# Optimization experiments

Measured on AMD Instinct MI355X. Metric: run time of the kernel, lower is better.

## Reference

```python
import jax, jax.numpy as jnp
import numpy as np

E = 1024
H = 16
DH = E // H
LN_EPS = 1e-5


def setup_inputs() -> dict:
    key = jax.random.key(0)
    ks = jax.random.split(key, 9)
    B, Lq, Lk = 8, 1024, 1024
    s = 0.02
    return {
        "query": jax.random.normal(ks[0], (B, Lq, E), jnp.float32),
        "key_t": jax.random.normal(ks[1], (B, Lk, E), jnp.float32),
        "value": jax.random.normal(ks[2], (B, Lk, E), jnp.float32),
        "in_proj_w": jax.random.normal(ks[3], (3 * E, E), jnp.float32) * s,
        "in_proj_b": jnp.zeros((3 * E,), jnp.float32),
        "out_proj_w": jax.random.normal(ks[4], (E, E), jnp.float32) * s,
        "out_proj_b": jnp.zeros((E,), jnp.float32),
        "ln_gamma": jnp.ones((E,), jnp.float32),
        "ln_beta": jnp.zeros((E,), jnp.float32),
    }


def _mha_cross(query, key_t, value, in_proj_w, in_proj_b, out_proj_w, out_proj_b,
               ln_gamma, ln_beta):
    B, Lq, _ = query.shape
    Lk = key_t.shape[1]
    wq, wk, wv = in_proj_w[:E], in_proj_w[E:2 * E], in_proj_w[2 * E:]
    bq, bk, bv = in_proj_b[:E], in_proj_b[E:2 * E], in_proj_b[2 * E:]
    # projections (torch Linear: x @ W^T + b)
    q = (query @ wq.T + bq).reshape(B, Lq, H, DH)
    k = (key_t @ wk.T + bk).reshape(B, Lk, H, DH)
    v = (value @ wv.T + bv).reshape(B, Lk, H, DH)
    scale = 1.0 / np.sqrt(DH).astype(np.float32)
    # unfused attention: explicit [B,H,Lq,Lk] scores (need_weights=True path)
    scores = jnp.einsum("bqhd,bkhd->bhqk", q, k) * scale
    probs = jax.nn.softmax(scores, axis=-1)
    attn = jnp.einsum("bhqk,bkhd->bqhd", probs, v).reshape(B, Lq, E)
    attn_out = attn @ out_proj_w.T + out_proj_b
    # averaged attention weights (average_attn_weights=True default)
    attn_weights = probs.mean(axis=1)  # [B, Lq, Lk]
    # residual + LayerNorm
    x = query + attn_out
    mu = x.mean(axis=-1, keepdims=True)
    var = x.var(axis=-1, keepdims=True)
    y = (x - mu) * jax.lax.rsqrt(var + LN_EPS) * ln_gamma + ln_beta
    return y, attn_weights


def reference(query, key_t, value, in_proj_w, in_proj_b, out_proj_w, out_proj_b,
              ln_gamma, ln_beta):
    return _mha_cross(query, key_t, value, in_proj_w, in_proj_b,
                      out_proj_w, out_proj_b, ln_gamma, ln_beta)
```

## Files before the change

kernel.cpp:

```cpp
#include <hip/hip_runtime.h>
#include <stdint.h>

#define E_DIM 1024
#define H_NUM 16
#define B_NUM 8
#define LQ 1024
#define LK 1024
#define MROWS (B_NUM * LQ)

typedef unsigned short u16;
typedef __attribute__((ext_vector_type(8))) short bf16x8;
typedef __attribute__((ext_vector_type(4))) short bf16x4;
typedef __attribute__((ext_vector_type(4))) float f32x4;
typedef bf16x8 __attribute__((may_alias)) bf16x8_ma;
typedef bf16x4 __attribute__((may_alias)) bf16x4_ma;
typedef f32x4 __attribute__((may_alias)) f32x4_ma;

typedef __attribute__((address_space(1))) const void* gas_ptr;
typedef __attribute__((address_space(3))) void* las_ptr;

__device__ __forceinline__ void gload16(const void* g, void* l) {
  __builtin_amdgcn_global_load_lds((gas_ptr)g, (las_ptr)l, 16, 0, 0);
}

__device__ __forceinline__ u16 f2bf(float f) {
  union { float f; uint32_t u; } c; c.f = f;
  return (u16)((c.u + 0x7FFFu + ((c.u >> 16) & 1u)) >> 16);
}

#define MFMA_BF16(a, b, c) __builtin_amdgcn_mfma_f32_16x16x32_bf16((a), (b), (c), 0, 0, 0)

#define SCALE_Q 0.18033688011112042f

__global__ __launch_bounds__(256) void cvt_f32_bf16(const float* __restrict__ src,
                                                    u16* __restrict__ dst, int n4) {
  int i = blockIdx.x * 256 + threadIdx.x;
  const int stride = gridDim.x * 256;
  for (; i < n4; i += stride) {
    float4 v = ((const float4*)src)[i];
    ushort4 o;
    o.x = f2bf(v.x); o.y = f2bf(v.y); o.z = f2bf(v.z); o.w = f2bf(v.w);
    ((ushort4*)dst)[i] = o;
  }
}

__global__ __launch_bounds__(256) void cvt3_f32_bf16(
    const float* __restrict__ a0, const float* __restrict__ a1, const float* __restrict__ a2,
    u16* __restrict__ o0, u16* __restrict__ o1, u16* __restrict__ o2, int n4) {
  const float* s = (blockIdx.y == 0) ? a0 : (blockIdx.y == 1 ? a1 : a2);
  u16* d = (blockIdx.y == 0) ? o0 : (blockIdx.y == 1 ? o1 : o2);
  int i = blockIdx.x * 256 + threadIdx.x;
  const int stride = gridDim.x * 256;
  for (; i < n4; i += stride) {
    float4 v = ((const float4*)s)[i];
    ushort4 o;
    o.x = f2bf(v.x); o.y = f2bf(v.y); o.z = f2bf(v.z); o.w = f2bf(v.w);
    ((ushort4*)d)[i] = o;
  }
}


#define BAR() __builtin_amdgcn_s_barrier()
#define LGKM0() do { asm volatile("s_waitcnt lgkmcnt(0)" ::: "memory"); \
                     __builtin_amdgcn_sched_barrier(0); } while (0)
#define LGKM8() asm volatile("s_waitcnt lgkmcnt(8)" ::: "memory")
#define VMC(n) asm volatile("s_waitcnt vmcnt(" n ")" ::: "memory")

#define STAGEH(mat, rowbase, kt, ldsoff)                                     \
  { const u16* _s = (mat) + (size_t)(rowbase) * E_DIM + (kt);                \
    gload16(_s + goff0, ldsv + (ldsoff) + wave * 1024);                      \
    gload16(_s + goff1, ldsv + (ldsoff) + 8192 + wave * 1024); }

#define READ_B(db)                                                           \
  _Pragma("unroll") for (int n = 0; n < 4; ++n) {                            \
    const int rgb = wn4 + n;                                                 \
    _Pragma("unroll") for (int ks = 0; ks < 2; ++ks)                         \
      bfr[n][ks] = *(const bf16x8_ma*)(ldsc + 65536 + (db) * 32768 +         \
          ((rgb >> 3) << 14) + (((rgb & 7) * 2 + ks) << 10) + lanebase);     \
  }

#define READ_A(db, q)                                                        \
  _Pragma("unroll") for (int jj = 0; jj < 2; ++jj) {                         \
    const int rga = 4 * (q) + 2 * jj + wm;                                   \
    _Pragma("unroll") for (int ks = 0; ks < 2; ++ks)                         \
      afr[jj][ks] = *(const bf16x8_ma*)(ldsc + (db) * 32768 +                \
          ((rga >> 3) << 14) + (((rga & 7) * 2 + ks) << 10) + lanebase);     \
  }

#define MMA(q)                                                               \
  __builtin_amdgcn_s_setprio(1);                                             \
  _Pragma("unroll") for (int jj = 0; jj < 2; ++jj)                           \
    _Pragma("unroll") for (int n = 0; n < 4; ++n)                            \
      _Pragma("unroll") for (int ks = 0; ks < 2; ++ks)                       \
        acc[2 * (q) + jj][n] =                                               \
            MFMA_BF16(afr[jj][ks], bfr[n][ks], acc[2 * (q) + jj][n]);        \
  __builtin_amdgcn_s_setprio(0);

template <int MODE>
__global__ __launch_bounds__(512, 2) void gemm256(
    const u16* __restrict__ A0, const u16* __restrict__ A1, const u16* __restrict__ A2,
    const u16* __restrict__ W, const float* __restrict__ bias,
    const float* __restrict__ resid,
    u16* __restrict__ outb, float* __restrict__ outf,
    int nwg_n, int nwg_m) {
  __shared__ u16 lds[65536];

  const int tid = threadIdx.x;
  const int wave = tid >> 6, lane = tid & 63;
  const int lr = lane & 15, lg = lane >> 4;
  const int wm = wave >> 2, wn4 = (wave & 3) * 4;

  const int cpx = (int)gridDim.x >> 3;
  const int bid = blockIdx.x;
  const int wg = (bid & 7) * cpx + (bid >> 3);
  const int n_i = wg % nwg_n;
  const int rest = wg / nwg_n;
  const int m_i = rest % nwg_m;
  const int z = rest / nwg_m;
  const int m0 = m_i * 256, n0 = n_i * 256;

  const u16* Az = (z == 0) ? A0 : (z == 1 ? A1 : A2);
  const u16* Wz = W + (size_t)z * E_DIM * E_DIM;
  const float* bs = bias + z * E_DIM;
  const float scale = (MODE == 0 && z == 0) ? SCALE_Q : 1.0f;

  int goff0, goff1;
  {
    const int X0 = wave * 1024 + lane * 16;
    const int L0 = X0 ^ (((X0 >> 9) & 1) << 5);
    goff0 = (((L0 >> 10) >> 1) * 16 + ((L0 >> 6) & 15)) * E_DIM +
            ((L0 >> 10) & 1) * 32 + ((L0 & 63) >> 1);
    const int X1 = 8192 + X0;
    const int L1 = X1 ^ (((X1 >> 9) & 1) << 5);
    goff1 = (((L1 >> 10) >> 1) * 16 + ((L1 >> 6) & 15)) * E_DIM +
            ((L1 >> 10) & 1) * 32 + ((L1 & 63) >> 1);
  }
  const char* ldsc = (const char*)lds;
  char* ldsv = (char*)lds;
  const int lanebase = lr * 64 + ((lg * 16) ^ ((lane & 8) << 2));

  const f32x4 fzero = {0.f, 0.f, 0.f, 0.f};
  f32x4 acc[8][4];
#pragma unroll
  for (int j = 0; j < 8; ++j)
#pragma unroll
    for (int n = 0; n < 4; ++n) acc[j][n] = fzero;

  STAGEH(Az, m0,       0,  0);
  STAGEH(Az, m0 + 128, 0,  16384);
  STAGEH(Wz, n0,       0,  65536);
  STAGEH(Wz, n0 + 128, 0,  65536 + 16384);
  STAGEH(Wz, n0,       64, 65536 + 32768);
  STAGEH(Wz, n0 + 128, 64, 65536 + 32768 + 16384);
  STAGEH(Az, m0,       64, 32768);
  VMC("6");
  BAR();

  bf16x8 bfr[4][2], afr[2][2];
#pragma unroll 1
  for (int i = 0; i < 8; ++i) {
    const int kt2 = i * 128 + 128;
    const bool nl = (i < 7);
    READ_B(0) READ_A(0, 0)
    STAGEH(Az, m0 + 128, i * 128 + 64, 32768 + 16384);
    LGKM8();
    BAR(); LGKM0();
    MMA(0)
    BAR();
    READ_A(0, 1)
    if (nl) STAGEH(Wz, n0, kt2, 65536);
    BAR(); LGKM0();
    MMA(1)
    BAR();
    READ_A(0, 2)
    if (nl) STAGEH(Az, m0, kt2, 0);
    BAR(); LGKM0();
    MMA(2)
    BAR();
    READ_A(0, 3)
    if (nl) {
      STAGEH(Wz, n0 + 128, kt2, 65536 + 16384);
      VMC("6");
    } else {
      VMC("0");
    }
    BAR(); LGKM0();
    MMA(3)
    BAR();
    READ_B(1) READ_A(1, 0)
    if (nl) STAGEH(Az, m0 + 128, kt2, 16384);
    LGKM8();
    BAR(); LGKM0();
    MMA(0)
    BAR();
    READ_A(1, 1)
    if (nl) STAGEH(Wz, n0, kt2 + 64, 65536 + 32768);
    BAR(); LGKM0();
    MMA(1)
    BAR();
    READ_A(1, 2)
    if (nl) STAGEH(Wz, n0 + 128, kt2 + 64, 65536 + 32768 + 16384);
    BAR(); LGKM0();
    MMA(2)
    BAR();
    READ_A(1, 3)
    if (nl) {
      STAGEH(Az, m0, kt2 + 64, 32768);
      VMC("6");
    }
    BAR(); LGKM0();
    MMA(3)
    BAR();
  }

  float bvv[4];
#pragma unroll
  for (int n = 0; n < 4; ++n) bvv[n] = bs[n0 + wn4 * 16 + n * 16 + lr];

  if (MODE == 0) {
    u16* Cb = outb + (size_t)z * (size_t)MROWS * E_DIM;
#pragma unroll
    for (int j = 0; j < 8; ++j) {
      const int rbase = m0 + (2 * j + wm) * 16 + lg * 4;
#pragma unroll
      for (int ii = 0; ii < 4; ++ii) {
        const size_t m = (size_t)(rbase + ii);
#pragma unroll
        for (int n = 0; n < 4; ++n) {
          const int nn = n0 + wn4 * 16 + n * 16 + lr;
          Cb[m * E_DIM + nn] = f2bf((acc[j][n][ii] + bvv[n]) * scale);
        }
      }
    }
  } else {
#pragma unroll
    for (int j = 0; j < 8; ++j) {
      const int rbase = m0 + (2 * j + wm) * 16 + lg * 4;
#pragma unroll
      for (int ii = 0; ii < 4; ++ii) {
        const size_t m = (size_t)(rbase + ii);
#pragma unroll
        for (int n = 0; n < 4; ++n) {
          const int nn = n0 + wn4 * 16 + n * 16 + lr;
          outf[m * E_DIM + nn] = acc[j][n][ii] + bvv[n] + resid[m * E_DIM + nn];
        }
      }
    }
  }
}

__global__ __launch_bounds__(256) void gemm128_out(
    const u16* __restrict__ A, const u16* __restrict__ W,
    const float* __restrict__ bias, const float* __restrict__ resid,
    float* __restrict__ outf, int nwg_n, int nwg_m) {
  __shared__ u16 As[128 * 64];
  __shared__ u16 Bs[128 * 64];

  const int tid = threadIdx.x;
  const int wave = tid >> 6;
  const int lane = tid & 63;
  const int lr = lane & 15, lg = lane >> 4;
  const int wr = wave >> 1, wc = wave & 1;

  const int cpx = (int)gridDim.x >> 3;
  const int bid = blockIdx.x;
  const int wg = (bid & 7) * cpx + (bid >> 3);
  const int n_i = wg % nwg_n;
  const int m_i = (wg / nwg_n) % nwg_m;

  const int m0 = m_i * 128;
  const int n0 = n_i * 128;

  const f32x4 fzero = {0.f, 0.f, 0.f, 0.f};
  f32x4 acc[4][4];
#pragma unroll
  for (int a = 0; a < 4; ++a)
#pragma unroll
    for (int b = 0; b < 4; ++b) acc[a][b] = fzero;

  const int lrow8 = lane >> 3;
  const int lcol8 = (lane & 7) * 8;

  for (int kt = 0; kt < E_DIM; kt += 64) {
#pragma unroll
    for (int i = 0; i < 4; ++i) {
      const int seg = i * 4 + wave;
      gload16(W + (size_t)(n0 + seg * 8 + lrow8) * E_DIM + kt + lcol8, &Bs[seg * 512]);
      gload16(A + (size_t)(m0 + seg * 8 + lrow8) * E_DIM + kt + lcol8, &As[seg * 512]);
    }
    __syncthreads();

#pragma unroll
    for (int kk = 0; kk < 64; kk += 32) {
      bf16x8 av[4], bv[4];
#pragma unroll
      for (int t = 0; t < 4; ++t)
        av[t] = *(const bf16x8*)&As[(wr * 64 + t * 16 + lr) * 64 + kk + lg * 8];
#pragma unroll
      for (int t = 0; t < 4; ++t)
        bv[t] = *(const bf16x8*)&Bs[(wc * 64 + t * 16 + lr) * 64 + kk + lg * 8];
#pragma unroll
      for (int mi = 0; mi < 4; ++mi)
#pragma unroll
        for (int ni = 0; ni < 4; ++ni)
          acc[mi][ni] = MFMA_BF16(av[mi], bv[ni], acc[mi][ni]);
    }
    __syncthreads();
  }

  float bvv[4];
#pragma unroll
  for (int ni = 0; ni < 4; ++ni) bvv[ni] = bias[n0 + wc * 64 + ni * 16 + lr];

#pragma unroll
  for (int mi = 0; mi < 4; ++mi) {
#pragma unroll
    for (int i = 0; i < 4; ++i) {
      const size_t m = (size_t)(m0 + wr * 64 + mi * 16 + lg * 4 + i);
#pragma unroll
      for (int ni = 0; ni < 4; ++ni) {
        const int n = n0 + wc * 64 + ni * 16 + lr;
        outf[m * E_DIM + n] = acc[mi][ni][i] + bvv[ni] + resid[m * E_DIM + n];
      }
    }
  }
}

__global__ __launch_bounds__(256) void transpose_v(const u16* __restrict__ Vb,
                                                   u16* __restrict__ Vtg) {
  __shared__ u16 T[64 * 264];
  const int tid = threadIdx.x;
  const int b = blockIdx.z, h = blockIdx.y;
  const int k0 = blockIdx.x * 256;
  const int bh = b * H_NUM + h;
  const int krow = tid >> 3;
  const int d0 = (tid & 7) * 8;
  const int jst = krow & 7;
#pragma unroll
  for (int it = 0; it < 8; ++it) {
    const int k = it * 32 + krow;
    bf16x8 v = *(const bf16x8*)&Vb[(size_t)(b * LK + k0 + k) * E_DIM + h * 64 + d0];
#pragma unroll
    for (int jj = 0; jj < 8; ++jj) {
      const int j = (jj + jst) & 7;
      T[(d0 + j) * 264 + k] = (u16)v[j];
    }
  }
  __syncthreads();
  const int d = tid >> 2;
  const int kk0 = (tid & 3) * 64;
  u16* orow = &Vtg[(size_t)(bh * 64 + d) * LK + k0 + kk0];
#pragma unroll
  for (int c = 0; c < 8; ++c)
    *(bf16x8*)&orow[c * 8] = *(const bf16x8*)&T[d * 264 + kk0 + c * 8];
}

__global__ __launch_bounds__(256) void attn_fwd(
    const u16* __restrict__ Qb, const u16* __restrict__ Kb, const u16* __restrict__ Vtg,
    u16* __restrict__ attnb, float* __restrict__ rden) {
  __shared__ u16 Ks[64 * 72];
  __shared__ u16 Vt[64 * 72];
  __shared__ u16 Pw[4][16 * 72];

  const int tid = threadIdx.x;
  const int wave = tid >> 6, lane = tid & 63;
  const int lr = lane & 15, lg = lane >> 4;

  const int bid = blockIdx.x;
  const int wg = (bid & 7) * 256 + (bid >> 3);
  const int qt = wg & 15;
  const int h = (wg >> 4) & 15;
  const int b = wg >> 8;
  const int bh = b * H_NUM + h;
  const int q0 = qt * 64;

  const size_t qoff = (size_t)(b * LQ + q0 + wave * 16 + lr) * E_DIM + h * 64;
  const bf16x8 qf0 = *(const bf16x8*)&Qb[qoff + lg * 8];
  const bf16x8 qf1 = *(const bf16x8*)&Qb[qoff + 32 + lg * 8];

  const f32x4 fzero = {0.f, 0.f, 0.f, 0.f};
  f32x4 ctx[4];
#pragma unroll
  for (int d = 0; d < 4; ++d) ctx[d] = fzero;
  float dnl = 0.f;

  const int sr = tid >> 2;
  const int sc = (tid & 3) * 16;
  const u16* Kg = &Kb[(size_t)(b * LK + sr) * E_DIM + h * 64 + sc];
  const u16* Vg = &Vtg[(size_t)(bh * 64 + sr) * LK + sc];

  bf16x8 kr0 = *(const bf16x8*)(Kg);
  bf16x8 kr1 = *(const bf16x8*)(Kg + 8);
  bf16x8 vr0 = *(const bf16x8*)(Vg);
  bf16x8 vr1 = *(const bf16x8*)(Vg + 8);
  *(bf16x8*)&Ks[sr * 72 + sc] = kr0; *(bf16x8*)&Ks[sr * 72 + sc + 8] = kr1;
  *(bf16x8*)&Vt[sr * 72 + sc] = vr0; *(bf16x8*)&Vt[sr * 72 + sc + 8] = vr1;

  for (int t = 0; t < 16; ++t) {
    __syncthreads();
    if (t < 15) {
      const int k1 = (t + 1) * 64;
      kr0 = *(const bf16x8*)(Kg + (size_t)k1 * E_DIM);
      kr1 = *(const bf16x8*)(Kg + (size_t)k1 * E_DIM + 8);
      vr0 = *(const bf16x8*)(Vg + k1);
      vr1 = *(const bf16x8*)(Vg + k1 + 8);
    }
#pragma unroll
    for (int kf = 0; kf < 4; ++kf) {
      const bf16x8 kb0 = *(const bf16x8*)&Ks[(kf * 16 + lr) * 72 + lg * 8];
      const bf16x8 kb1 = *(const bf16x8*)&Ks[(kf * 16 + lr) * 72 + 32 + lg * 8];
      f32x4 s = fzero;
      s = MFMA_BF16(kb0, qf0, s);
      s = MFMA_BF16(kb1, qf1, s);
      const float p0 = exp2f(s[0]), p1 = exp2f(s[1]);
      const float p2 = exp2f(s[2]), p3 = exp2f(s[3]);
      dnl += (p0 + p1) + (p2 + p3);
      bf16x4 w;
      w[0] = (short)f2bf(p0); w[1] = (short)f2bf(p1);
      w[2] = (short)f2bf(p2); w[3] = (short)f2bf(p3);
      *(bf16x4_ma*)&Pw[wave][lr * 72 + kf * 16 + lg * 4] = w;
    }
    const bf16x8 pa0 = *(const bf16x8_ma*)&Pw[wave][lr * 72 + lg * 8];
    const bf16x8 pa1 = *(const bf16x8_ma*)&Pw[wave][lr * 72 + 32 + lg * 8];
#pragma unroll
    for (int df = 0; df < 4; ++df) {
      const bf16x8 vb0 = *(const bf16x8*)&Vt[(df * 16 + lr) * 72 + lg * 8];
      const bf16x8 vb1 = *(const bf16x8*)&Vt[(df * 16 + lr) * 72 + 32 + lg * 8];
      ctx[df] = MFMA_BF16(pa0, vb0, ctx[df]);
      ctx[df] = MFMA_BF16(pa1, vb1, ctx[df]);
    }
    __syncthreads();
    if (t < 15) {
      *(bf16x8*)&Ks[sr * 72 + sc] = kr0; *(bf16x8*)&Ks[sr * 72 + sc + 8] = kr1;
      *(bf16x8*)&Vt[sr * 72 + sc] = vr0; *(bf16x8*)&Vt[sr * 72 + sc + 8] = vr1;
    }
  }

  dnl += __shfl_xor(dnl, 16, 64);
  dnl += __shfl_xor(dnl, 32, 64);
  if (lane < 16) rden[(size_t)bh * LQ + q0 + wave * 16 + lane] = 0.0625f / dnl;
  float dnv[4];
#pragma unroll
  for (int i = 0; i < 4; ++i) dnv[i] = __shfl(dnl, lg * 4 + i, 64);

#pragma unroll
  for (int i = 0; i < 4; ++i) {
    const float inv = 1.0f / dnv[i];
    const int q = q0 + wave * 16 + lg * 4 + i;
    const size_t orow = (size_t)(b * LQ + q) * E_DIM + h * 64;
#pragma unroll
    for (int df = 0; df < 4; ++df)
      attnb[orow + df * 16 + lr] = f2bf(ctx[df][i] * inv);
  }
}

__global__ __launch_bounds__(256, 2) void attn_wts(
    const u16* __restrict__ Qb, const u16* __restrict__ Kb,
    const float* __restrict__ rden, float* __restrict__ aw) {
  __shared__ u16 Ks2[2][128 * 72];
  __shared__ u16 Qs[128 * 72];

  const int tid = threadIdx.x;
  const int wave = tid >> 6, lane = tid & 63;
  const int lr = lane & 15, lg = lane >> 4;
  const int wq = wave >> 1, wk = wave & 1;

  const int bid = blockIdx.x;
  const int wg = (bid & 7) * 64 + (bid >> 3);
  const int q0 = (wg & 7) * 128;
  const int k0 = ((wg >> 3) & 7) * 128;
  const int b = wg >> 6;

  const f32x4 fzero = {0.f, 0.f, 0.f, 0.f};
  f32x4 acc[4][4];
#pragma unroll
  for (int t = 0; t < 4; ++t)
#pragma unroll
    for (int j = 0; j < 4; ++j) acc[t][j] = fzero;

  const int sr = tid >> 1;
  const int sc = (tid & 1) * 32;
  const u16* Kg = &Kb[(size_t)(b * LK + k0 + sr) * E_DIM + sc];
  const u16* Qg = &Qb[(size_t)(b * LQ + q0 + sr) * E_DIM + sc];
  const float* dg = &rden[(size_t)(b * H_NUM) * LQ + q0 + wq * 64 + lr];

  bf16x8 kr[4], qr[4];
#pragma unroll
  for (int c = 0; c < 4; ++c) kr[c] = *(const bf16x8*)(Kg + c * 8);
#pragma unroll
  for (int c = 0; c < 4; ++c) qr[c] = *(const bf16x8*)(Qg + c * 8);
#pragma unroll
  for (int c = 0; c < 4; ++c) *(bf16x8*)&Ks2[0][sr * 72 + sc + c * 8] = kr[c];

  for (int h = 0; h < H_NUM; ++h) {
    __syncthreads();
#pragma unroll
    for (int c = 0; c < 4; ++c) *(bf16x8*)&Qs[sr * 72 + sc + c * 8] = qr[c];
    __syncthreads();

    if (h < 15) {
#pragma unroll
      for (int c = 0; c < 4; ++c) kr[c] = *(const bf16x8*)(Kg + (h + 1) * 64 + c * 8);
#pragma unroll
      for (int c = 0; c < 4; ++c) qr[c] = *(const bf16x8*)(Qg + (h + 1) * 64 + c * 8);
    }
    float rd[4];
#pragma unroll
    for (int j = 0; j < 4; ++j) rd[j] = dg[(size_t)h * LQ + j * 16];

    const u16* Kbuf = &Ks2[h & 1][0];
    bf16x8 kb[4][2];
#pragma unroll
    for (int t = 0; t < 4; ++t) {
      const int row = wk * 64 + t * 16 + lr;
      kb[t][0] = *(const bf16x8*)&Kbuf[row * 72 + lg * 8];
      kb[t][1] = *(const bf16x8*)&Kbuf[row * 72 + 32 + lg * 8];
    }
#pragma unroll
    for (int j = 0; j < 4; ++j) {
      const int qrow = wq * 64 + j * 16 + lr;
      const bf16x8 qf0 = *(const bf16x8*)&Qs[qrow * 72 + lg * 8];
      const bf16x8 qf1 = *(const bf16x8*)&Qs[qrow * 72 + 32 + lg * 8];
#pragma unroll
      for (int t = 0; t < 4; ++t) {
        f32x4 s = fzero;
        s = MFMA_BF16(kb[t][0], qf0, s);
        s = MFMA_BF16(kb[t][1], qf1, s);
#pragma unroll
        for (int i = 0; i < 4; ++i)
          acc[t][j][i] += exp2f(s[i]) * rd[j];
      }
    }

    if (h < 15) {
      u16* Kw = &Ks2[(h + 1) & 1][0];
#pragma unroll
      for (int c = 0; c < 4; ++c) *(bf16x8*)&Kw[sr * 72 + sc + c * 8] = kr[c];
    }
  }

#pragma unroll
  for (int j = 0; j < 4; ++j) {
    const size_t orow = (size_t)(b * LQ + q0 + wq * 64 + j * 16 + lr) * LK;
#pragma unroll
    for (int t = 0; t < 4; ++t)
      *(f32x4_ma*)&aw[orow + k0 + wk * 64 + t * 16 + lg * 4] = acc[t][j];
  }
}

__global__ __launch_bounds__(256) void ln_kernel(float* __restrict__ xy,
                                                 const float* __restrict__ gamma,
                                                 const float* __restrict__ beta) {
  __shared__ float ls[4], ls2[4];
  const int row = blockIdx.x;
  const int tid = threadIdx.x;
  float4* xr = (float4*)(xy + (size_t)row * E_DIM);
  float4 v = xr[tid];
  float s = v.x + v.y + v.z + v.w;
  float s2 = v.x * v.x + v.y * v.y + v.z * v.z + v.w * v.w;
#pragma unroll
  for (int off = 32; off >= 1; off >>= 1) {
    s += __shfl_xor(s, off, 64);
    s2 += __shfl_xor(s2, off, 64);
  }
  const int wave = tid >> 6, lane = tid & 63;
  if (lane == 0) { ls[wave] = s; ls2[wave] = s2; }
  __syncthreads();
  s = ls[0] + ls[1] + ls[2] + ls[3];
  s2 = ls2[0] + ls2[1] + ls2[2] + ls2[3];
  const float mu = s * (1.0f / E_DIM);
  const float var = s2 * (1.0f / E_DIM) - mu * mu;
  const float rs = rsqrtf(var + 1e-5f);
  const float4 g = ((const float4*)gamma)[tid];
  const float4 bt = ((const float4*)beta)[tid];
  float4 o;
  o.x = (v.x - mu) * rs * g.x + bt.x;
  o.y = (v.y - mu) * rs * g.y + bt.y;
  o.z = (v.z - mu) * rs * g.z + bt.z;
  o.w = (v.w - mu) * rs * g.w + bt.w;
  xr[tid] = o;
}

extern "C" void kernel_launch(void* const* d_in, const int* in_sizes, int n_in,
                              void* d_out, int out_size, void* d_ws, size_t ws_size,
                              hipStream_t stream) {
  (void)in_sizes; (void)n_in; (void)out_size; (void)ws_size;
  const float* query     = (const float*)d_in[0];
  const float* key_t     = (const float*)d_in[1];
  const float* value     = (const float*)d_in[2];
  const float* in_proj_b = (const float*)d_in[4];
  const float* out_proj_b = (const float*)d_in[6];
  const float* ln_gamma  = (const float*)d_in[7];
  const float* ln_beta   = (const float*)d_in[8];

  float* y  = (float*)d_out;
  float* aw = y + (size_t)B_NUM * LQ * E_DIM;

  const size_t SZ = (size_t)B_NUM * LQ * E_DIM;
  u16* ws    = (u16*)d_ws;
  u16* Qb    = ws;
  u16* Kb    = ws + SZ;
  u16* Vb    = ws + 2 * SZ;
  u16* attnb = ws + 3 * SZ;
  u16* wqkvb = ws + 4 * SZ;
  u16* woutb = wqkvb + 3 * E_DIM * E_DIM;
  float* rden = (float*)(wqkvb + 4 * (size_t)E_DIM * E_DIM);

  u16* Xq  = (u16*)aw;
  u16* Xk  = Xq + SZ;
  u16* Xv  = (u16*)y;
  u16* Vtg = (u16*)y;

  cvt_f32_bf16<<<3072, 256, 0, stream>>>((const float*)d_in[3], wqkvb, (3 * E_DIM * E_DIM) / 4);
  cvt_f32_bf16<<<1024, 256, 0, stream>>>((const float*)d_in[5], woutb, (E_DIM * E_DIM) / 4);
  cvt3_f32_bf16<<<dim3(2048, 3), 256, 0, stream>>>(query, key_t, value, Xq, Xk, Xv, (int)(SZ / 4));

  gemm256<0><<<384, 512, 0, stream>>>(
      Xq, Xk, Xv, wqkvb, in_proj_b, nullptr, Qb, nullptr, 4, 32);

  transpose_v<<<dim3(4, 16, 8), 256, 0, stream>>>(Vb, Vtg);

  attn_fwd<<<2048, 256, 0, stream>>>(Qb, Kb, Vtg, attnb, rden);

  attn_wts<<<512, 256, 0, stream>>>(Qb, Kb, rden, aw);

  gemm128_out<<<512, 256, 0, stream>>>(attnb, woutb, out_proj_b, query, y, 8, 64);

  ln_kernel<<<8192, 256, 0, stream>>>(y, ln_gamma, ln_beta);
}
```

Measured before the change: 272.5 us.

## Route output projection through 256-tile GEMM and pack P to bf16 via perm

Drops the dedicated 128x128 output-projection GEMM and reuses the existing 256-tile GEMM template in its residual/fp32-output mode, launched with 128 blocks of 512 threads. The aim is more data reuse per tile and a single well-tuned GEMM path. In the attention kernel, probabilities are now packed to bf16 by truncating with one byte-permute per pair instead of rounding each value separately, which cuts VALU work. The truncation changes rounding (toward zero instead of nearest-even), and 128 blocks may underfill a GPU with many CUs.

After: 269.2 us. No clear change (-1.2%).

```diff
diff --git a/kernel.cpp b/kernel.cpp
--- a/kernel.cpp
+++ b/kernel.cpp
@@ -12,9 +12,11 @@
 typedef __attribute__((ext_vector_type(8))) short bf16x8;
 typedef __attribute__((ext_vector_type(4))) short bf16x4;
 typedef __attribute__((ext_vector_type(4))) float f32x4;
+typedef __attribute__((ext_vector_type(2))) unsigned int u32x2;
 typedef bf16x8 __attribute__((may_alias)) bf16x8_ma;
 typedef bf16x4 __attribute__((may_alias)) bf16x4_ma;
 typedef f32x4 __attribute__((may_alias)) f32x4_ma;
+typedef u32x2 __attribute__((may_alias)) u32x2_ma;
 
 typedef __attribute__((address_space(1))) const void* gas_ptr;
 typedef __attribute__((address_space(3))) void* las_ptr;
@@ -28,9 +30,14 @@
   return (u16)((c.u + 0x7FFFu + ((c.u >> 16) & 1u)) >> 16);
 }
 
+__device__ __forceinline__ uint32_t pack2bf(float lo, float hi) {
+  return __builtin_amdgcn_perm(__float_as_uint(hi), __float_as_uint(lo), 0x07060302u);
+}
+
 #define MFMA_BF16(a, b, c) __builtin_amdgcn_mfma_f32_16x16x32_bf16((a), (b), (c), 0, 0, 0)
 
 #define SCALE_Q 0.18033688011112042f
+
 
 __global__ __launch_bounds__(256) void cvt_f32_bf16(const float* __restrict__ src,
                                                     u16* __restrict__ dst, int n4) {
@@ -249,83 +256,6 @@
   }
 }
 
-__global__ __launch_bounds__(256) void gemm128_out(
-    const u16* __restrict__ A, const u16* __restrict__ W,
-    const float* __restrict__ bias, const float* __restrict__ resid,
-    float* __restrict__ outf, int nwg_n, int nwg_m) {
-  __shared__ u16 As[128 * 64];
-  __shared__ u16 Bs[128 * 64];
-
-  const int tid = threadIdx.x;
-  const int wave = tid >> 6;
-  const int lane = tid & 63;
-  const int lr = lane & 15, lg = lane >> 4;
-  const int wr = wave >> 1, wc = wave & 1;
-
-  const int cpx = (int)gridDim.x >> 3;
-  const int bid = blockIdx.x;
-  const int wg = (bid & 7) * cpx + (bid >> 3);
-  const int n_i = wg % nwg_n;
-  const int m_i = (wg / nwg_n) % nwg_m;
-
-  const int m0 = m_i * 128;
-  const int n0 = n_i * 128;
-
-  const f32x4 fzero = {0.f, 0.f, 0.f, 0.f};
-  f32x4 acc[4][4];
-#pragma unroll
-  for (int a = 0; a < 4; ++a)
-#pragma unroll
-    for (int b = 0; b < 4; ++b) acc[a][b] = fzero;
-
-  const int lrow8 = lane >> 3;
-  const int lcol8 = (lane & 7) * 8;
-
-  for (int kt = 0; kt < E_DIM; kt += 64) {
-#pragma unroll
-    for (int i = 0; i < 4; ++i) {
-      const int seg = i * 4 + wave;
-      gload16(W + (size_t)(n0 + seg * 8 + lrow8) * E_DIM + kt + lcol8, &Bs[seg * 512]);
-      gload16(A + (size_t)(m0 + seg * 8 + lrow8) * E_DIM + kt + lcol8, &As[seg * 512]);
-    }
-    __syncthreads();
-
-#pragma unroll
-    for (int kk = 0; kk < 64; kk += 32) {
-      bf16x8 av[4], bv[4];
-#pragma unroll
-      for (int t = 0; t < 4; ++t)
-        av[t] = *(const bf16x8*)&As[(wr * 64 + t * 16 + lr) * 64 + kk + lg * 8];
-#pragma unroll
-      for (int t = 0; t < 4; ++t)
-        bv[t] = *(const bf16x8*)&Bs[(wc * 64 + t * 16 + lr) * 64 + kk + lg * 8];
-#pragma unroll
-      for (int mi = 0; mi < 4; ++mi)
-#pragma unroll
-        for (int ni = 0; ni < 4; ++ni)
-          acc[mi][ni] = MFMA_BF16(av[mi], bv[ni], acc[mi][ni]);
-    }
-    __syncthreads();
-  }
-
-  float bvv[4];
-#pragma unroll
-  for (int ni = 0; ni < 4; ++ni) bvv[ni] = bias[n0 + wc * 64 + ni * 16 + lr];
-
-#pragma unroll
-  for (int mi = 0; mi < 4; ++mi) {
-#pragma unroll
-    for (int i = 0; i < 4; ++i) {
-      const size_t m = (size_t)(m0 + wr * 64 + mi * 16 + lg * 4 + i);
-#pragma unroll
-      for (int ni = 0; ni < 4; ++ni) {
-        const int n = n0 + wc * 64 + ni * 16 + lr;
-        outf[m * E_DIM + n] = acc[mi][ni][i] + bvv[ni] + resid[m * E_DIM + n];
-      }
-    }
-  }
-}
-
 __global__ __launch_bounds__(256) void transpose_v(const u16* __restrict__ Vb,
                                                    u16* __restrict__ Vtg) {
   __shared__ u16 T[64 * 264];
@@ -415,10 +345,10 @@
       const float p0 = exp2f(s[0]), p1 = exp2f(s[1]);
       const float p2 = exp2f(s[2]), p3 = exp2f(s[3]);
       dnl += (p0 + p1) + (p2 + p3);
-      bf16x4 w;
-      w[0] = (short)f2bf(p0); w[1] = (short)f2bf(p1);
-      w[2] = (short)f2bf(p2); w[3] = (short)f2bf(p3);
-      *(bf16x4_ma*)&Pw[wave][lr * 72 + kf * 16 + lg * 4] = w;
+      u32x2 w;
+      w[0] = pack2bf(p0, p1);
+      w[1] = pack2bf(p2, p3);
+      *(u32x2_ma*)&Pw[wave][lr * 72 + kf * 16 + lg * 4] = w;
     }
     const bf16x8 pa0 = *(const bf16x8_ma*)&Pw[wave][lr * 72 + lg * 8];
     const bf16x8 pa1 = *(const bf16x8_ma*)&Pw[wave][lr * 72 + 32 + lg * 8];
@@ -624,7 +554,8 @@
 
   attn_wts<<<512, 256, 0, stream>>>(Qb, Kb, rden, aw);
 
-  gemm128_out<<<512, 256, 0, stream>>>(attnb, woutb, out_proj_b, query, y, 8, 64);
+  gemm256<1><<<128, 512, 0, stream>>>(
+      attnb, attnb, attnb, woutb, out_proj_b, query, nullptr, y, 4, 32);
 
   ln_kernel<<<8192, 256, 0, stream>>>(y, ln_gamma, ln_beta);
 }
```
